# Kernel optimization log

Hardware: AMD Instinct MI355X
Metric: run time of the kernel (lower is better)

Reference implementation:

```python
import jax, jax.numpy as jnp
import numpy as np
from jax import lax

DIM = 512
HEADS = 4
NUM_KEYS = 256
TOPK = 32
DIM_HEAD = 128
B, T = 2, 2048
DIM_QUERY = DIM_HEAD * HEADS * 2


def setup_inputs() -> dict:
    key = jax.random.key(0)
    k_x, k_wq, k_keys, k_vals = jax.random.split(key, 4)
    x = jax.random.normal(k_x, (B, T, DIM), dtype=jnp.float32)
    # nn.Linear(dim, dim_query, bias=False): weight [out, in]
    wq = jax.random.normal(k_wq, (DIM_QUERY, DIM), dtype=jnp.float32) / np.sqrt(DIM)
    # LayerNorm(dim_head) params
    ln_g = jnp.ones((DIM_HEAD,), dtype=jnp.float32)
    ln_b = jnp.zeros((DIM_HEAD,), dtype=jnp.float32)
    # product keys: [heads, num_keys, 2, dim_head], init std = 1/sqrt(dim_head)
    keys = jax.random.normal(k_keys, (HEADS, NUM_KEYS, 2, DIM_HEAD), dtype=jnp.float32) / np.sqrt(DIM_HEAD)
    # EmbeddingBag values: [num_keys**2, dim], init std = 1/sqrt(dim)
    values = jax.random.normal(k_vals, (NUM_KEYS * NUM_KEYS, DIM), dtype=jnp.float32) / np.sqrt(DIM)
    return {"x": x, "wq": wq, "ln_g": ln_g, "ln_b": ln_b, "keys": keys, "values": values}


def _layernorm(q, g, b, eps=1e-5):
    mu = q.mean(-1, keepdims=True)
    var = ((q - mu) ** 2).mean(-1, keepdims=True)
    return (q - mu) * lax.rsqrt(var + eps) * g + b


def reference(x, wq, ln_g, ln_b, keys, values):
    b, t, _ = x.shape
    h, dh, nk, k = HEADS, DIM_HEAD, NUM_KEYS, TOPK
    # queries: [b, t, 2*h*dh] -> [b, t, p, h, dh] (p outer per '(p h d)')
    q = jnp.einsum('btc,qc->btq', x, wq).reshape(b, t, 2, h, dh)
    q = _layernorm(q, ln_g, ln_b)
    # dots: einsum('p b t h d, h n p d -> b t h p n')
    dots = jnp.einsum('btphd,hnpd->bthpn', q, keys)
    # first top-k along num_keys, per sub-key half
    scores, indices = lax.top_k(dots, k)              # [b, t, h, 2, k]
    sx, sy = scores[..., 0, :], scores[..., 1, :]
    ix, iy = indices[..., 0, :], indices[..., 1, :]
    # cross-product of candidates: [b, t, h, k*k]
    all_scores = (sx[..., :, None] + sy[..., None, :]).reshape(b, t, h, k * k)
    all_indices = (ix[..., :, None] * nk + iy[..., None, :]).reshape(b, t, h, k * k)
    # second top-k over the k^2 cross terms
    final_scores, fidx = lax.top_k(all_scores, k)     # [b, t, h, k]
    value_indices = jnp.take_along_axis(all_indices, fidx, axis=-1)
    attn = jax.nn.softmax(final_scores, axis=-1)
    # EmbeddingBag(mode='sum', per_sample_weights): weighted gather-sum over h*k rows
    vidx = value_indices.reshape(b * t, h * k)
    w = attn.reshape(b * t, h * k)
    out = jnp.einsum('nk,nkd->nd', w, values[vidx])   # [(b t), dim]
    return out.reshape(b, t, DIM)
```

## Files before the change

### kernel.cpp

```cpp
#include <hip/hip_runtime.h>
#include <hip/hip_bf16.h>

#define NT    4096
#define DIMC  512
#define DQ    1024
#define NH    4
#define DH    128
#define NKEY  256
#define TK    32

typedef unsigned long long u64;
typedef unsigned int u32;

__global__ __launch_bounds__(256) void k_qproj_ln(
    const float* __restrict__ x, const float* __restrict__ wq,
    const float* __restrict__ ln_g, const float* __restrict__ ln_b,
    float* __restrict__ qn) {
  const int bm = blockIdx.x * 64;
  const int nb = blockIdx.y;
  const int n0 = nb * 128;
  const int tid = threadIdx.x;
  const int tx = tid & 15;
  const int ty = tid >> 4;

  __shared__ __align__(16) float As[16][68];
  __shared__ __align__(16) float Bs[16][130];

  float acc[4][8];
#pragma unroll
  for (int r = 0; r < 4; ++r)
#pragma unroll
    for (int c = 0; c < 8; ++c) acc[r][c] = 0.0f;

  for (int k0 = 0; k0 < DIMC; k0 += 16) {
    {
      int row = tid >> 2, kg = tid & 3;
      float4 v = *reinterpret_cast<const float4*>(
          &x[(size_t)(bm + row) * DIMC + k0 + kg * 4]);
      As[kg * 4 + 0][row] = v.x; As[kg * 4 + 1][row] = v.y;
      As[kg * 4 + 2][row] = v.z; As[kg * 4 + 3][row] = v.w;
    }
#pragma unroll
    for (int it = 0; it < 2; ++it) {
      int idx = it * 256 + tid;
      int rn = idx >> 2, kg = idx & 3;
      float4 v = *reinterpret_cast<const float4*>(
          &wq[(size_t)(n0 + rn) * DIMC + k0 + kg * 4]);
      Bs[kg * 4 + 0][rn] = v.x; Bs[kg * 4 + 1][rn] = v.y;
      Bs[kg * 4 + 2][rn] = v.z; Bs[kg * 4 + 3][rn] = v.w;
    }
    __syncthreads();
#pragma unroll
    for (int kk = 0; kk < 16; ++kk) {
      float4 a4 = *reinterpret_cast<const float4*>(&As[kk][ty * 4]);
      float2 bp0 = *reinterpret_cast<const float2*>(&Bs[kk][2 * tx]);
      float2 bp1 = *reinterpret_cast<const float2*>(&Bs[kk][2 * tx + 32]);
      float2 bp2 = *reinterpret_cast<const float2*>(&Bs[kk][2 * tx + 64]);
      float2 bp3 = *reinterpret_cast<const float2*>(&Bs[kk][2 * tx + 96]);
      float af[4] = {a4.x, a4.y, a4.z, a4.w};
      float bf[8] = {bp0.x, bp0.y, bp1.x, bp1.y, bp2.x, bp2.y, bp3.x, bp3.y};
#pragma unroll
      for (int r = 0; r < 4; ++r)
#pragma unroll
        for (int c = 0; c < 8; ++c)
          acc[r][c] = fmaf(af[r], bf[c], acc[r][c]);
    }
    __syncthreads();
  }

  double gg[8], bb[8];
#pragma unroll
  for (int c = 0; c < 8; ++c) {
    int d = 2 * tx + 32 * (c >> 1) + (c & 1);
    gg[c] = (double)ln_g[d]; bb[c] = (double)ln_b[d];
  }
#pragma unroll
  for (int r = 0; r < 4; ++r) {
    double qf[8];
#pragma unroll
    for (int c = 0; c < 8; ++c) qf[c] = (double)acc[r][c];
    double s = 0.0;
#pragma unroll
    for (int c = 0; c < 8; ++c) s += qf[c];
#pragma unroll
    for (int m = 1; m < 16; m <<= 1) s += __shfl_xor(s, m, 64);
    double mu = s * (1.0 / 128.0);
    double vs = 0.0;
#pragma unroll
    for (int c = 0; c < 8; ++c) { double d = qf[c] - mu; vs += d * d; }
#pragma unroll
    for (int m = 1; m < 16; m <<= 1) vs += __shfl_xor(vs, m, 64);
    double rstd = 1.0 / sqrt(vs * (1.0 / 128.0) + 1e-5);
    float* o = &qn[(size_t)(bm + ty * 4 + r) * DQ + n0];
#pragma unroll
    for (int cp = 0; cp < 4; ++cp) {
      float2 st;
      st.x = (float)((qf[2 * cp] - mu) * rstd * gg[2 * cp] + bb[2 * cp]);
      st.y = (float)((qf[2 * cp + 1] - mu) * rstd * gg[2 * cp + 1] + bb[2 * cp + 1]);
      *reinterpret_cast<float2*>(&o[2 * tx + 32 * cp]) = st;
    }
  }
}

__global__ __launch_bounds__(256) void k_dots(
    const float* __restrict__ qn, const float* __restrict__ keys,
    float* __restrict__ sc) {
  const int t0 = blockIdx.x * 32;
  const int p = blockIdx.y;
  const int h = blockIdx.z;
  const int qoff = p * 512 + h * 128;
  const int tid = threadIdx.x;
  const int tx = tid & 31;
  const int ty = tid >> 5;

  __shared__ __align__(16) float Asf[32][36];
  __shared__ __align__(16) float Bs[32][258];

  float acc[4][8];
#pragma unroll
  for (int r = 0; r < 4; ++r)
#pragma unroll
    for (int c = 0; c < 8; ++c) acc[r][c] = 0.0f;

  for (int k0 = 0; k0 < DH; k0 += 32) {
    {
      int m = tid >> 3, kg = tid & 7;
      float4 v = *reinterpret_cast<const float4*>(
          &qn[(size_t)(t0 + m) * DQ + qoff + k0 + kg * 4]);
      Asf[kg * 4 + 0][m] = v.x; Asf[kg * 4 + 1][m] = v.y;
      Asf[kg * 4 + 2][m] = v.z; Asf[kg * 4 + 3][m] = v.w;
    }
#pragma unroll
    for (int it = 0; it < 8; ++it) {
      int idx = it * 256 + tid;
      int n = idx >> 3, kg = idx & 7;
      float4 v = *reinterpret_cast<const float4*>(
          &keys[(size_t)((h * NKEY + n) * 2 + p) * DH + k0 + kg * 4]);
      Bs[kg * 4 + 0][n] = v.x; Bs[kg * 4 + 1][n] = v.y;
      Bs[kg * 4 + 2][n] = v.z; Bs[kg * 4 + 3][n] = v.w;
    }
    __syncthreads();
#pragma unroll
    for (int kk = 0; kk < 32; ++kk) {
      float4 a4 = *reinterpret_cast<const float4*>(&Asf[kk][ty * 4]);
      float2 b0 = *reinterpret_cast<const float2*>(&Bs[kk][2 * tx]);
      float2 b1 = *reinterpret_cast<const float2*>(&Bs[kk][2 * tx + 64]);
      float2 b2 = *reinterpret_cast<const float2*>(&Bs[kk][2 * tx + 128]);
      float2 b3 = *reinterpret_cast<const float2*>(&Bs[kk][2 * tx + 192]);
      float af[4] = {a4.x, a4.y, a4.z, a4.w};
      float bf[8] = {b0.x, b0.y, b1.x, b1.y, b2.x, b2.y, b3.x, b3.y};
#pragma unroll
      for (int r = 0; r < 4; ++r)
#pragma unroll
        for (int c = 0; c < 8; ++c)
          acc[r][c] = fmaf(af[r], bf[c], acc[r][c]);
    }
    __syncthreads();
  }

#pragma unroll
  for (int r = 0; r < 4; ++r) {
    float* o = &sc[(((size_t)h * NT + (t0 + ty * 4 + r)) * 2 + p) * NKEY];
#pragma unroll
    for (int cp = 0; cp < 4; ++cp) {
      float2 st;
      st.x = acc[r][2 * cp];
      st.y = acc[r][2 * cp + 1];
      *reinterpret_cast<float2*>(&o[2 * tx + 64 * cp]) = st;
    }
  }
}

__device__ __forceinline__ u32 ford(float f) {
  u32 u = __float_as_uint(f);
  return u ^ (0x80000000u | (u32)((int)u >> 31));
}
__device__ __forceinline__ float funord(u32 o) {
  u32 b = (o & 0x80000000u) ? (o ^ 0x80000000u) : ~o;
  return __uint_as_float(b);
}

__device__ const short cand_tbl[128] = {
  0,1,2,3,4,5,6,7,8,9,10,11,12,13,14,15,16,17,18,19,20,21,22,23,24,25,26,27,28,29,30,31,
  32,33,34,35,36,37,38,39,40,41,42,43,44,45,46,47,
  64,65,66,67,68,69,70,71,72,73,
  96,97,98,99,100,101,102,103,
  128,129,130,131,132,133,
  160,161,162,163,164,
  192,193,194,195,
  224,225,226,227,
  256,257,258, 288,289,290,
  320,321, 352,353, 384,385, 416,417, 448,449, 480,481,
  512,544,576,608,640,672,704,736,768,800,832,864,896,928,960,992,
  -1,-1,-1,-1,-1,-1,-1,-1,-1
};

template <int NS>
__device__ __forceinline__ void sort32(u64* key, int i) {
#pragma unroll
  for (int k = 2; k <= 32; k <<= 1) {
#pragma unroll
    for (int j = k >> 1; j > 0; j >>= 1) {
      bool up = ((i & k) == 0);
#pragma unroll
      for (int r = 0; r < NS; ++r) {
        u64 o = __shfl_xor(key[r], j, 64);
        u64 mx = key[r] > o ? key[r] : o;
        u64 mn = key[r] < o ? key[r] : o;
        key[r] = (((i & j) == 0) == up) ? mx : mn;
      }
    }
  }
}

__device__ __forceinline__ u64 bmerge32(u64 a, int i) {
#pragma unroll
  for (int j = 16; j > 0; j >>= 1) {
    u64 o = __shfl_xor(a, j, 64);
    u64 mx = a > o ? a : o;
    u64 mn = a < o ? a : o;
    a = ((i & j) == 0) ? mx : mn;
  }
  return a;
}

__device__ __forceinline__ u64 mergehalf(u64 a, int i) {
  u64 o = __shfl_xor(a, 63, 64);
  a = a > o ? a : o;
  return bmerge32(a, i);
}

__device__ __forceinline__ u64 mergeslots(u64 a, u64 b, int i) {
  u64 o = __shfl_xor(b, 31, 64);
  a = a > o ? a : o;
  return bmerge32(a, i);
}

__global__ __launch_bounds__(256) void k_topk(
    const float* __restrict__ sc, float* __restrict__ wout,
    int* __restrict__ vout) {
  const int t = blockIdx.x;
  const int lane = threadIdx.x & 63;
  const int h = threadIdx.x >> 6;
  const int i = lane & 31;

  u64 X, Y;
#pragma unroll
  for (int p = 0; p < 2; ++p) {
    const float* base = &sc[(((size_t)h * NT + t) * 2 + p) * NKEY];
    u64 key[4];
#pragma unroll
    for (int r = 0; r < 4; ++r) {
      int n = r * 64 + lane;
      key[r] = ((u64)ford(base[n]) << 32) | (u64)(0xFFFFFFFFu - (u32)n);
    }
    sort32<4>(key, i);
#pragma unroll
    for (int r = 0; r < 4; ++r) key[r] = mergehalf(key[r], i);
    u64 m01 = mergeslots(key[0], key[1], i);
    u64 m23 = mergeslots(key[2], key[3], i);
    u64 m = mergeslots(m01, m23, i);
    if (p == 0) X = m; else Y = m;
  }

  float xs = funord((u32)(X >> 32));
  float ys = funord((u32)(Y >> 32));
  u32 xn = 0xFFFFFFFFu - (u32)X;
  u32 yn = 0xFFFFFFFFu - (u32)Y;

  u64 s2[2];
#pragma unroll
  for (int r = 0; r < 2; ++r) {
    int ce = (int)cand_tbl[r * 64 + lane];
    int ci = (ce >= 0) ? (ce >> 5) : 0;
    int cj = (ce >= 0) ? (ce & 31) : 0;
    float sum = __shfl(xs, ci, 64) + __shfl(ys, cj, 64);
    u64 kk = ((u64)ford(sum) << 32) | (u64)(0xFFFFFFFFu - (u32)ce);
    s2[r] = (ce >= 0) ? kk : 0ull;
  }
  sort32<2>(s2, i);
#pragma unroll
  for (int r = 0; r < 2; ++r) s2[r] = mergehalf(s2[r], i);
  u64 F = mergeslots(s2[0], s2[1], i);

  float fs = funord((u32)(F >> 32));
  u32 c = 0xFFFFFFFFu - (u32)F;
  double m0 = (double)__shfl(fs, 0, 64);
  double e = exp((double)fs - m0);
  double ssum = e;
#pragma unroll
  for (int m = 1; m < 32; m <<= 1) ssum += __shfl_xor(ssum, m, 64);
  int ci = (int)(c >> 5), cj = (int)(c & 31);
  int nx = (int)__shfl(xn, ci, 64);
  int ny = (int)__shfl(yn, cj, 64);
  if (lane < 32) {
    wout[(size_t)(t * NH + h) * TK + lane] = (float)(e / ssum);
    vout[(size_t)(t * NH + h) * TK + lane] = nx * NKEY + ny;
  }
}

__device__ __forceinline__ unsigned short bfr(float f) {
  u32 u = __float_as_uint(f);
  return (unsigned short)((u + 0x7fffu + ((u >> 16) & 1u)) >> 16);
}

__global__ __launch_bounds__(256) void k_cvt(
    const float* __restrict__ v, unsigned short* __restrict__ vb) {
  size_t i = (size_t)blockIdx.x * 256 + threadIdx.x;
  const size_t stride = (size_t)4096 * 256;
#pragma unroll
  for (int it = 0; it < 8; ++it) {
    size_t g = i + (size_t)it * stride;
    float4 a = reinterpret_cast<const float4*>(v)[g];
    ushort4 o;
    o.x = bfr(a.x); o.y = bfr(a.y); o.z = bfr(a.z); o.w = bfr(a.w);
    reinterpret_cast<ushort4*>(vb)[g] = o;
  }
}

__global__ __launch_bounds__(256) void k_gather(
    const unsigned short* __restrict__ vb, const float* __restrict__ w,
    const int* __restrict__ vidx, float* __restrict__ out) {
  const int t = blockIdx.x;
  const int tid = threadIdx.x;
  const int wid = tid >> 6;
  const int lane = tid & 63;
  __shared__ float lw[128];
  __shared__ int lv[128];
  __shared__ float part[4][512];
  if (tid < 128) {
    lw[tid] = w[(size_t)t * 128 + tid];
    lv[tid] = vidx[(size_t)t * 128 + tid];
  }
  __syncthreads();
  float acc[8];
#pragma unroll
  for (int e = 0; e < 8; ++e) acc[e] = 0.f;
  const int jb = wid * 32;
#pragma unroll 8
  for (int k = 0; k < 32; ++k) {
    float wj = lw[jb + k];
    const uint4 v = *reinterpret_cast<const uint4*>(
        &vb[(size_t)lv[jb + k] * DIMC + lane * 8]);
    acc[0] = fmaf(wj, __uint_as_float(v.x << 16), acc[0]);
    acc[1] = fmaf(wj, __uint_as_float(v.x & 0xffff0000u), acc[1]);
    acc[2] = fmaf(wj, __uint_as_float(v.y << 16), acc[2]);
    acc[3] = fmaf(wj, __uint_as_float(v.y & 0xffff0000u), acc[3]);
    acc[4] = fmaf(wj, __uint_as_float(v.z << 16), acc[4]);
    acc[5] = fmaf(wj, __uint_as_float(v.z & 0xffff0000u), acc[5]);
    acc[6] = fmaf(wj, __uint_as_float(v.w << 16), acc[6]);
    acc[7] = fmaf(wj, __uint_as_float(v.w & 0xffff0000u), acc[7]);
  }
  float4* pp = reinterpret_cast<float4*>(&part[wid][lane * 8]);
  pp[0] = make_float4(acc[0], acc[1], acc[2], acc[3]);
  pp[1] = make_float4(acc[4], acc[5], acc[6], acc[7]);
  __syncthreads();
  int d = tid * 2;
  float2 o;
  o.x = (part[0][d]     + part[1][d])     + (part[2][d]     + part[3][d]);
  o.y = (part[0][d + 1] + part[1][d + 1]) + (part[2][d + 1] + part[3][d + 1]);
  *reinterpret_cast<float2*>(&out[(size_t)t * DIMC + d]) = o;
}

extern "C" void kernel_launch(void* const* d_in, const int* in_sizes, int n_in,
                              void* d_out, int out_size, void* d_ws, size_t ws_size,
                              hipStream_t stream) {
  const float* x      = (const float*)d_in[0];
  const float* wq     = (const float*)d_in[1];
  const float* ln_g   = (const float*)d_in[2];
  const float* ln_b   = (const float*)d_in[3];
  const float* keys   = (const float*)d_in[4];
  const float* values = (const float*)d_in[5];
  float* out = (float*)d_out;

  char* ws = (char*)d_ws;
  unsigned short* vb = (unsigned short*)ws;
  float* qn  = (float*)ws;
  float* sc  = (float*)(ws + 16777216);
  float* wv  = (float*)(ws + 67108864);
  int*   vi  = (int*)(ws + 67108864 + 2097152);

  k_qproj_ln<<<dim3(64, 8), 256, 0, stream>>>(x, wq, ln_g, ln_b, qn);
  k_dots<<<dim3(128, 2, 4), 256, 0, stream>>>(qn, keys, sc);
  k_topk<<<dim3(4096), 256, 0, stream>>>(sc, wv, vi);
  k_cvt<<<dim3(4096), 256, 0, stream>>>(values, vb);
  k_gather<<<dim3(4096), 256, 0, stream>>>(vb, wv, vi, out);
}
```

Baseline: 468.0 us.

## Co-schedule values bf16 conversion with query projection and enlarge GEMM tiles

Folds the values fp32-to-bf16 conversion into the query-projection launch as extra blocks, so the memory-bound conversion runs alongside the compute-bound projection when the workspace is large enough to keep the buffers separate. It also doubles the per-thread row tile (8x8 accumulators) in both the projection and dots kernels, which halves the grid sizes and improves register reuse. The costs are higher register pressure, fewer blocks for occupancy, and a fallback path that depends on workspace size.

```diff
diff --git a/kernel.cpp b/kernel.cpp
--- a/kernel.cpp
+++ b/kernel.cpp
@@ -12,29 +12,49 @@
 typedef unsigned long long u64;
 typedef unsigned int u32;
 
-__global__ __launch_bounds__(256) void k_qproj_ln(
+__device__ __forceinline__ unsigned short bfr(float f) {
+  u32 u = __float_as_uint(f);
+  return (unsigned short)((u + 0x7fffu + ((u >> 16) & 1u)) >> 16);
+}
+
+__global__ __launch_bounds__(256) void k_qproj_cvt(
     const float* __restrict__ x, const float* __restrict__ wq,
     const float* __restrict__ ln_g, const float* __restrict__ ln_b,
-    float* __restrict__ qn) {
-  const int bm = blockIdx.x * 64;
-  const int nb = blockIdx.y;
-  const int n0 = nb * 128;
+    float* __restrict__ qn, const float* __restrict__ vals,
+    unsigned short* __restrict__ vb, int nCvt) {
   const int tid = threadIdx.x;
+
+  if (blockIdx.x >= 256) {
+    const size_t nthr = (size_t)nCvt * 256;
+    size_t g0 = (size_t)(blockIdx.x - 256) * 256 + tid;
+    for (size_t g = g0; g < 8388608ull; g += nthr) {
+      float4 a = reinterpret_cast<const float4*>(vals)[g];
+      ushort4 o;
+      o.x = bfr(a.x); o.y = bfr(a.y); o.z = bfr(a.z); o.w = bfr(a.w);
+      reinterpret_cast<ushort4*>(vb)[g] = o;
+    }
+    return;
+  }
+
+  const int bm = (blockIdx.x & 31) * 128;
+  const int n0 = (blockIdx.x >> 5) * 128;
   const int tx = tid & 15;
   const int ty = tid >> 4;
 
-  __shared__ __align__(16) float As[16][68];
+  __shared__ __align__(16) float As[16][132];
   __shared__ __align__(16) float Bs[16][130];
 
-  float acc[4][8];
-#pragma unroll
-  for (int r = 0; r < 4; ++r)
+  float acc[8][8];
+#pragma unroll
+  for (int r = 0; r < 8; ++r)
 #pragma unroll
     for (int c = 0; c < 8; ++c) acc[r][c] = 0.0f;
 
   for (int k0 = 0; k0 < DIMC; k0 += 16) {
-    {
-      int row = tid >> 2, kg = tid & 3;
+#pragma unroll
+    for (int it = 0; it < 2; ++it) {
+      int idx = it * 256 + tid;
+      int row = idx >> 2, kg = idx & 3;
       float4 v = *reinterpret_cast<const float4*>(
           &x[(size_t)(bm + row) * DIMC + k0 + kg * 4]);
       As[kg * 4 + 0][row] = v.x; As[kg * 4 + 1][row] = v.y;
@@ -52,15 +72,16 @@
     __syncthreads();
 #pragma unroll
     for (int kk = 0; kk < 16; ++kk) {
-      float4 a4 = *reinterpret_cast<const float4*>(&As[kk][ty * 4]);
+      float4 alo = *reinterpret_cast<const float4*>(&As[kk][ty * 8]);
+      float4 ahi = *reinterpret_cast<const float4*>(&As[kk][ty * 8 + 4]);
       float2 bp0 = *reinterpret_cast<const float2*>(&Bs[kk][2 * tx]);
       float2 bp1 = *reinterpret_cast<const float2*>(&Bs[kk][2 * tx + 32]);
       float2 bp2 = *reinterpret_cast<const float2*>(&Bs[kk][2 * tx + 64]);
       float2 bp3 = *reinterpret_cast<const float2*>(&Bs[kk][2 * tx + 96]);
-      float af[4] = {a4.x, a4.y, a4.z, a4.w};
+      float af[8] = {alo.x, alo.y, alo.z, alo.w, ahi.x, ahi.y, ahi.z, ahi.w};
       float bf[8] = {bp0.x, bp0.y, bp1.x, bp1.y, bp2.x, bp2.y, bp3.x, bp3.y};
 #pragma unroll
-      for (int r = 0; r < 4; ++r)
+      for (int r = 0; r < 8; ++r)
 #pragma unroll
         for (int c = 0; c < 8; ++c)
           acc[r][c] = fmaf(af[r], bf[c], acc[r][c]);
@@ -75,7 +96,7 @@
     gg[c] = (double)ln_g[d]; bb[c] = (double)ln_b[d];
   }
 #pragma unroll
-  for (int r = 0; r < 4; ++r) {
+  for (int r = 0; r < 8; ++r) {
     double qf[8];
 #pragma unroll
     for (int c = 0; c < 8; ++c) qf[c] = (double)acc[r][c];
@@ -91,7 +112,7 @@
 #pragma unroll
     for (int m = 1; m < 16; m <<= 1) vs += __shfl_xor(vs, m, 64);
     double rstd = 1.0 / sqrt(vs * (1.0 / 128.0) + 1e-5);
-    float* o = &qn[(size_t)(bm + ty * 4 + r) * DQ + n0];
+    float* o = &qn[(size_t)(bm + ty * 8 + r) * DQ + n0];
 #pragma unroll
     for (int cp = 0; cp < 4; ++cp) {
       float2 st;
@@ -105,7 +126,7 @@
 __global__ __launch_bounds__(256) void k_dots(
     const float* __restrict__ qn, const float* __restrict__ keys,
     float* __restrict__ sc) {
-  const int t0 = blockIdx.x * 32;
+  const int t0 = blockIdx.x * 64;
   const int p = blockIdx.y;
   const int h = blockIdx.z;
   const int qoff = p * 512 + h * 128;
@@ -113,18 +134,20 @@
   const int tx = tid & 31;
   const int ty = tid >> 5;
 
-  __shared__ __align__(16) float Asf[32][36];
+  __shared__ __align__(16) float Asf[32][68];
   __shared__ __align__(16) float Bs[32][258];
 
-  float acc[4][8];
-#pragma unroll
-  for (int r = 0; r < 4; ++r)
+  float acc[8][8];
+#pragma unroll
+  for (int r = 0; r < 8; ++r)
 #pragma unroll
     for (int c = 0; c < 8; ++c) acc[r][c] = 0.0f;
 
   for (int k0 = 0; k0 < DH; k0 += 32) {
-    {
-      int m = tid >> 3, kg = tid & 7;
+#pragma unroll
+    for (int it = 0; it < 2; ++it) {
+      int idx = it * 256 + tid;
+      int m = idx >> 3, kg = idx & 7;
       float4 v = *reinterpret_cast<const float4*>(
           &qn[(size_t)(t0 + m) * DQ + qoff + k0 + kg * 4]);
       Asf[kg * 4 + 0][m] = v.x; Asf[kg * 4 + 1][m] = v.y;
@@ -142,15 +165,16 @@
     __syncthreads();
 #pragma unroll
     for (int kk = 0; kk < 32; ++kk) {
-      float4 a4 = *reinterpret_cast<const float4*>(&Asf[kk][ty * 4]);
+      float4 alo = *reinterpret_cast<const float4*>(&Asf[kk][ty * 8]);
+      float4 ahi = *reinterpret_cast<const float4*>(&Asf[kk][ty * 8 + 4]);
       float2 b0 = *reinterpret_cast<const float2*>(&Bs[kk][2 * tx]);
       float2 b1 = *reinterpret_cast<const float2*>(&Bs[kk][2 * tx + 64]);
       float2 b2 = *reinterpret_cast<const float2*>(&Bs[kk][2 * tx + 128]);
       float2 b3 = *reinterpret_cast<const float2*>(&Bs[kk][2 * tx + 192]);
-      float af[4] = {a4.x, a4.y, a4.z, a4.w};
+      float af[8] = {alo.x, alo.y, alo.z, alo.w, ahi.x, ahi.y, ahi.z, ahi.w};
       float bf[8] = {b0.x, b0.y, b1.x, b1.y, b2.x, b2.y, b3.x, b3.y};
 #pragma unroll
-      for (int r = 0; r < 4; ++r)
+      for (int r = 0; r < 8; ++r)
 #pragma unroll
         for (int c = 0; c < 8; ++c)
           acc[r][c] = fmaf(af[r], bf[c], acc[r][c]);
@@ -159,8 +183,8 @@
   }
 
 #pragma unroll
-  for (int r = 0; r < 4; ++r) {
-    float* o = &sc[(((size_t)h * NT + (t0 + ty * 4 + r)) * 2 + p) * NKEY];
+  for (int r = 0; r < 8; ++r) {
+    float* o = &sc[(((size_t)h * NT + (t0 + ty * 8 + r)) * 2 + p) * NKEY];
 #pragma unroll
     for (int cp = 0; cp < 4; ++cp) {
       float2 st;
@@ -297,11 +321,6 @@
     wout[(size_t)(t * NH + h) * TK + lane] = (float)(e / ssum);
     vout[(size_t)(t * NH + h) * TK + lane] = nx * NKEY + ny;
   }
-}
-
-__device__ __forceinline__ unsigned short bfr(float f) {
-  u32 u = __float_as_uint(f);
-  return (unsigned short)((u + 0x7fffu + ((u >> 16) & 1u)) >> 16);
 }
 
 __global__ __launch_bounds__(256) void k_cvt(
@@ -374,15 +393,28 @@
   float* out = (float*)d_out;
 
   char* ws = (char*)d_ws;
-  unsigned short* vb = (unsigned short*)ws;
-  float* qn  = (float*)ws;
-  float* sc  = (float*)(ws + 16777216);
-  float* wv  = (float*)(ws + 67108864);
-  int*   vi  = (int*)(ws + 67108864 + 2097152);
-
-  k_qproj_ln<<<dim3(64, 8), 256, 0, stream>>>(x, wq, ln_g, ln_b, qn);
-  k_dots<<<dim3(128, 2, 4), 256, 0, stream>>>(qn, keys, sc);
+  const bool overlap = ws_size >= (size_t)116 * 1024 * 1024;
+
+  float* qn = (float*)ws;
+  float* sc = (float*)(ws + (16ull << 20));
+  unsigned short* vb;
+  float* wv;
+  int*   vi;
+  if (overlap) {
+    vb = (unsigned short*)(ws + (48ull << 20));
+    wv = (float*)(ws + (112ull << 20));
+    vi = (int*)(ws + (114ull << 20));
+  } else {
+    vb = (unsigned short*)ws;
+    wv = (float*)(ws + (64ull << 20));
+    vi = (int*)(ws + (66ull << 20));
+  }
+
+  const int nCvt = overlap ? 1024 : 0;
+  k_qproj_cvt<<<dim3(256 + nCvt), 256, 0, stream>>>(
+      x, wq, ln_g, ln_b, qn, values, vb, nCvt);
+  k_dots<<<dim3(64, 2, 4), 256, 0, stream>>>(qn, keys, sc);
   k_topk<<<dim3(4096), 256, 0, stream>>>(sc, wv, vi);
-  k_cvt<<<dim3(4096), 256, 0, stream>>>(values, vb);
+  if (!overlap) k_cvt<<<dim3(4096), 256, 0, stream>>>(values, vb);
   k_gather<<<dim3(4096), 256, 0, stream>>>(vb, wv, vi, out);
 }
```

New measurement: 430.3 us. 8.0% less time.
